# Performance work log

Measured on AMD Instinct MI355X. Metric: run time of the kernel, lower is better.

## Reference

```python
import jax, jax.numpy as jnp
import numpy as np

D_MODEL = 2048
D_FF = 8192
N_EXPERTS = 4
B, S = 2, 2048


def setup_inputs() -> dict:
    key = jax.random.key(0)
    ks = jax.random.split(key, 6)
    scale = 0.02
    return {
        "hidden_states": jax.random.normal(ks[0], (B, S, D_MODEL), dtype=jnp.float32),
        "Wr": jax.random.normal(ks[1], (D_MODEL, N_EXPERTS), dtype=jnp.float32) * scale,
        "br": jnp.zeros((N_EXPERTS,), dtype=jnp.float32),
        "Wg": jax.random.normal(ks[2], (N_EXPERTS, D_MODEL, D_FF), dtype=jnp.float32) * scale,
        "Wu": jax.random.normal(ks[3], (N_EXPERTS, D_MODEL, D_FF), dtype=jnp.float32) * scale,
        "Wd": jax.random.normal(ks[4], (N_EXPERTS, D_FF, D_MODEL), dtype=jnp.float32) * scale,
    }


def reference(hidden_states, Wr, br, Wg, Wu, Wd):
    b, s, d = hidden_states.shape
    x = hidden_states.reshape(-1, d)  # [T, d]

    # Router: top-1 over softmax probabilities
    logits = x @ Wr + br                      # [T, E]
    probs = jax.nn.softmax(logits, axis=-1)   # [T, E]
    top_w, top_idx = jax.lax.top_k(probs, 1)  # [T, 1], [T, 1]

    # Mistral gated MLP per expert, computed densely then selected (same math
    # as masked gather -> expert MLP -> masked_scatter with top-1 routing).
    g = jnp.einsum('td,edf->tef', x, Wg)      # [T, E, f]
    u = jnp.einsum('td,edf->tef', x, Wu)      # [T, E, f]
    h = jax.nn.silu(g) * u                    # [T, E, f]
    y = jnp.einsum('tef,efd->ted', h, Wd)     # [T, E, d]

    sel = jnp.take_along_axis(y, top_idx[:, :, None], axis=1)[:, 0]  # [T, d]
    out = sel * top_w                          # scale by top-1 routing weight
    return out.reshape(b, s, d)
```

## Files before the change

### kernel.cpp

```cpp
#include <hip/hip_runtime.h>

#define T_TOK 4096
#define DM 2048
#define DF 8192
#define NE 4
#define BM 256
#define BN 64
#define GBN 128
#define GBK 64
#define G2BK 32
#define BKO 32
#define MAX_TILES 20
#define PADROWS 256
#define LDK (BKO + 8)

typedef __attribute__((ext_vector_type(8))) short short8;
typedef __attribute__((ext_vector_type(4))) float f32x4;

__device__ __forceinline__ unsigned short f2bf(float f) {
  unsigned int u = __float_as_uint(f);
  u += 0x7fffu + ((u >> 16) & 1u);
  return (unsigned short)(u >> 16);
}

__device__ __forceinline__ void gld_lds16(const unsigned short* g, unsigned short* l) {
  __builtin_amdgcn_global_load_lds(
      (const __attribute__((address_space(1))) unsigned int*)g,
      (__attribute__((address_space(3))) unsigned int*)l, 16, 0, 0);
}

__global__ __launch_bounds__(256) void router_kernel(
    const float* __restrict__ x, const float* __restrict__ Wr,
    const float* __restrict__ br, int* __restrict__ top_idx,
    float* __restrict__ top_w, int* __restrict__ counts) {
  int tok = (blockIdx.x * blockDim.x + threadIdx.x) >> 6;
  int lane = threadIdx.x & 63;
  if (tok >= T_TOK) return;
  const float* xr = x + (size_t)tok * DM;
  float s0 = 0.f, s1 = 0.f, s2 = 0.f, s3 = 0.f;
  for (int j = lane; j < DM; j += 64) {
    float xv = xr[j];
    float4 w = *(const float4*)(Wr + (size_t)j * NE);
    s0 += xv * w.x; s1 += xv * w.y; s2 += xv * w.z; s3 += xv * w.w;
  }
#pragma unroll
  for (int off = 32; off > 0; off >>= 1) {
    s0 += __shfl_xor(s0, off);
    s1 += __shfl_xor(s1, off);
    s2 += __shfl_xor(s2, off);
    s3 += __shfl_xor(s3, off);
  }
  if (lane == 0) {
    float l[NE] = {s0 + br[0], s1 + br[1], s2 + br[2], s3 + br[3]};
    int bi = 0; float bm = l[0];
#pragma unroll
    for (int e = 1; e < NE; e++) if (l[e] > bm) { bm = l[e]; bi = e; }
    float s = 0.f;
#pragma unroll
    for (int e = 0; e < NE; e++) s += __expf(l[e] - bm);
    top_idx[tok] = bi;
    top_w[tok] = 1.0f / s;
    atomicAdd(&counts[bi], 1);
  }
}

__global__ void scan_kernel(const int* __restrict__ counts, int* __restrict__ offs,
                            int* __restrict__ cursors, int* __restrict__ tiles) {
  if (threadIdx.x != 0 || blockIdx.x != 0) return;
  int offv[NE + 1];
  offv[0] = 0;
  for (int e = 0; e < NE; e++) offv[e + 1] = offv[e] + counts[e];
  for (int e = 0; e <= NE; e++) offs[e] = offv[e];
  for (int e = 0; e < NE; e++) cursors[e] = offv[e];
  int nt = 0;
  for (int e = 0; e < NE; e++) {
    int c = counts[e];
    for (int s = 0; s < c; s += BM) {
      tiles[nt * 3 + 0] = e;
      tiles[nt * 3 + 1] = offv[e] + s;
      tiles[nt * 3 + 2] = (c - s < BM) ? (c - s) : BM;
      nt++;
    }
  }
  for (; nt < MAX_TILES; nt++) {
    tiles[nt * 3 + 0] = 0; tiles[nt * 3 + 1] = 0; tiles[nt * 3 + 2] = 0;
  }
}

__global__ __launch_bounds__(256) void scatter_kernel(
    const int* __restrict__ top_idx, int* __restrict__ cursors,
    int* __restrict__ sorted) {
  int t = blockIdx.x * blockDim.x + threadIdx.x;
  if (t >= T_TOK) return;
  int e = top_idx[t];
  int p = atomicAdd(&cursors[e], 1);
  sorted[p] = t;
}

__global__ __launch_bounds__(256) void gather_x_kernel(
    const float* __restrict__ x, const int* __restrict__ sorted,
    unsigned short* __restrict__ xs) {
  const int row = blockIdx.x;
  const int t = threadIdx.x;
  unsigned short* orow = xs + (size_t)row * DM + (t << 3);
  if (row >= T_TOK) {
    short8 z = (short8){0,0,0,0,0,0,0,0};
    *(short8*)orow = z;
    return;
  }
  const float* irow = x + (size_t)sorted[row] * DM + (t << 3);
  float4 a = *(const float4*)irow;
  float4 b = *(const float4*)(irow + 4);
  short8 p;
  p[0] = (short)f2bf(a.x); p[1] = (short)f2bf(a.y);
  p[2] = (short)f2bf(a.z); p[3] = (short)f2bf(a.w);
  p[4] = (short)f2bf(b.x); p[5] = (short)f2bf(b.y);
  p[6] = (short)f2bf(b.z); p[7] = (short)f2bf(b.w);
  *(short8*)orow = p;
}

__global__ __launch_bounds__(256) void transpose_cvt_kernel(
    const float* __restrict__ in, unsigned short* __restrict__ out, int R, int C) {
  __shared__ float tile[64][68];
  const size_t eo = (size_t)blockIdx.z * (size_t)R * (size_t)C;
  const float* inp = in + eo;
  unsigned short* outp = out + eo;
  const int r0 = blockIdx.y << 6, c0 = blockIdx.x << 6;
  const int t = threadIdx.x;
  const int lrow = t >> 4, lcol = (t & 15) << 2;
#pragma unroll
  for (int i = 0; i < 4; i++) {
    float4 v = *(const float4*)(inp + (size_t)(r0 + (i << 4) + lrow) * C + c0 + lcol);
    *(float4*)&tile[(i << 4) + lrow][lcol] = v;
  }
  __syncthreads();
  const int gg = t & 7, cc = t >> 3;
#pragma unroll
  for (int cp = 0; cp < 2; cp++) {
    int c = cc + (cp << 5);
    short8 pv;
#pragma unroll
    for (int i = 0; i < 8; i++) pv[i] = (short)f2bf(tile[(gg << 3) + i][c]);
    *(short8*)(outp + (size_t)(c0 + c) * R + r0 + (gg << 3)) = pv;
  }
}

__global__ __launch_bounds__(512, 2) void gemm1_bf16_kernel(
    const unsigned short* __restrict__ xs, const unsigned short* __restrict__ wg,
    const unsigned short* __restrict__ wu, const int* __restrict__ tiles,
    unsigned short* __restrict__ hbuf) {
  const int slot = blockIdx.x;
  const int e = tiles[slot * 3 + 0];
  const int row0 = tiles[slot * 3 + 1];
  const int nvalid = tiles[slot * 3 + 2];
  if (nvalid == 0) return;
  const int n0 = blockIdx.y * GBN;

  __shared__ __align__(16) unsigned short As[2][BM * GBK];
  __shared__ __align__(16) unsigned short Bg[2][GBN * GBK];
  __shared__ __align__(16) unsigned short Bu[2][GBN * GBK];

  const int t = threadIdx.x;
  const int w = t >> 6, lane = t & 63;
  const int l3 = lane >> 3;
  const int swz = (lane & 7) ^ l3;
  const int lr = lane & 15;
  const int wm = w >> 2, wn = w & 3;

  const unsigned short* wge = wg + (size_t)e * DM * DF;
  const unsigned short* wue = wu + (size_t)e * DM * DF;

  const unsigned short* sA = xs + (size_t)(row0 + (w << 6) + l3) * DM + (swz << 3);
  const unsigned short* sBg = wge + (size_t)(n0 + ((w - 4) << 6) + l3) * DM + (swz << 3);
  const unsigned short* sBu = wue + (size_t)(n0 + ((w - 6) << 6) + l3) * DM + (swz << 3);

  f32x4 accg[8][2], accu[8][2];
#pragma unroll
  for (int mi = 0; mi < 8; mi++)
#pragma unroll
    for (int ni = 0; ni < 2; ni++) {
      accg[mi][ni] = (f32x4){0.f, 0.f, 0.f, 0.f};
      accu[mi][ni] = (f32x4){0.f, 0.f, 0.f, 0.f};
    }

#define G1_STAGE(B, K0)                                                        \
  do {                                                                         \
    if (w < 4) {                                                               \
      unsigned short* d = &As[B][(w << 6) << 6];                               \
      _Pragma("unroll")                                                        \
      for (int j = 0; j < 8; j++)                                              \
        gld_lds16(sA + (size_t)(j << 3) * DM + (K0), d + (j << 9));            \
    } else if (w < 6) {                                                        \
      unsigned short* d = &Bg[B][((w - 4) << 6) << 6];                         \
      _Pragma("unroll")                                                        \
      for (int j = 0; j < 8; j++)                                              \
        gld_lds16(sBg + (size_t)(j << 3) * DM + (K0), d + (j << 9));           \
    } else {                                                                   \
      unsigned short* d = &Bu[B][((w - 6) << 6) << 6];                         \
      _Pragma("unroll")                                                        \
      for (int j = 0; j < 8; j++)                                              \
        gld_lds16(sBu + (size_t)(j << 3) * DM + (K0), d + (j << 9));           \
    }                                                                          \
  } while (0)

#define G1_COMPUTE(B)                                                          \
  do {                                                                         \
    _Pragma("unroll")                                                          \
    for (int h = 0; h < 2; h++) {                                              \
      const int gq = (h << 2) + (lane >> 4);                                   \
      const int g = gq ^ (lr & 7);                                             \
      short8 af[8], bgf[2], buf2[2];                                           \
      _Pragma("unroll")                                                        \
      for (int mi = 0; mi < 8; mi++) {                                         \
        int row = (wm << 7) + (mi << 4) + lr;                                  \
        af[mi] = *(const short8*)&As[B][(row << 6) + (g << 3)];                \
      }                                                                        \
      _Pragma("unroll")                                                        \
      for (int ni = 0; ni < 2; ni++) {                                         \
        int row = (wn << 5) + (ni << 4) + lr;                                  \
        bgf[ni]  = *(const short8*)&Bg[B][(row << 6) + (g << 3)];              \
        buf2[ni] = *(const short8*)&Bu[B][(row << 6) + (g << 3)];              \
      }                                                                        \
      _Pragma("unroll")                                                        \
      for (int mi = 0; mi < 8; mi++)                                           \
        _Pragma("unroll")                                                      \
        for (int ni = 0; ni < 2; ni++) {                                       \
          accg[mi][ni] = __builtin_amdgcn_mfma_f32_16x16x32_bf16(              \
              af[mi], bgf[ni], accg[mi][ni], 0, 0, 0);                         \
          accu[mi][ni] = __builtin_amdgcn_mfma_f32_16x16x32_bf16(              \
              af[mi], buf2[ni], accu[mi][ni], 0, 0, 0);                        \
        }                                                                      \
    }                                                                          \
  } while (0)

  const int NK = DM / GBK;
  int cur = 0;
  G1_STAGE(0, 0);
  __syncthreads();
  for (int kt = 0; kt < NK - 1; ++kt) {
    G1_STAGE(cur ^ 1, (kt + 1) * GBK);
    G1_COMPUTE(cur);
    __syncthreads();
    cur ^= 1;
  }
  G1_COMPUTE(cur);

  const int l4 = (lane >> 4) << 2;
#pragma unroll
  for (int mi = 0; mi < 8; mi++) {
#pragma unroll
    for (int r = 0; r < 4; r++) {
      int lrow = (wm << 7) + (mi << 4) + l4 + r;
      if (lrow < nvalid) {
        size_t base = (size_t)(row0 + lrow) * DF + n0 + (wn << 5) + lr;
#pragma unroll
        for (int ni = 0; ni < 2; ni++) {
          float gv = accg[mi][ni][r];
          float uv = accu[mi][ni][r];
          float hv = (gv / (1.f + __expf(-gv))) * uv;
          hbuf[base + (ni << 4)] = f2bf(hv);
        }
      }
    }
  }
#undef G1_STAGE
#undef G1_COMPUTE
}

__global__ __launch_bounds__(512, 4) void gemm2_bf16_kernel(
    const unsigned short* __restrict__ hbuf, const unsigned short* __restrict__ wd,
    const int* __restrict__ tiles, const int* __restrict__ sorted,
    const float* __restrict__ topw, float* __restrict__ out) {
  const int slot = blockIdx.x;
  const int e = tiles[slot * 3 + 0];
  const int row0 = tiles[slot * 3 + 1];
  const int nvalid = tiles[slot * 3 + 2];
  if (nvalid == 0) return;
  const int n0 = blockIdx.y * GBN;

  __shared__ __align__(16) unsigned short As[2][BM * G2BK];
  __shared__ __align__(16) unsigned short Bs[2][GBN * G2BK];

  const int t = threadIdx.x;
  const int w = t >> 6, lane = t & 63;
  const int lr = lane & 15;
  const int wm = w >> 2, wn = w & 3;

  const int srow = lane >> 2;
  const int sg = (lane & 3) ^ ((lane >> 3) & 3);

  const unsigned short* wde = wd + (size_t)e * DM * DF;
  const unsigned short* sA = hbuf + (size_t)(row0 + (w << 6) + srow) * DF + (sg << 3);
  const unsigned short* sB = wde + (size_t)(n0 + ((w - 4) << 5) + srow) * DF + (sg << 3);

  f32x4 acc[8][2];
#pragma unroll
  for (int mi = 0; mi < 8; mi++)
#pragma unroll
    for (int ni = 0; ni < 2; ni++) acc[mi][ni] = (f32x4){0.f, 0.f, 0.f, 0.f};

#define G2_STAGE(B_, K0)                                                       \
  do {                                                                         \
    if (w < 4) {                                                               \
      _Pragma("unroll")                                                        \
      for (int j = 0; j < 4; j++)                                              \
        gld_lds16(sA + (size_t)(j << 4) * DF + (K0),                           \
                  &As[B_][((w << 2) + j) << 9]);                               \
    } else {                                                                   \
      _Pragma("unroll")                                                        \
      for (int j = 0; j < 2; j++)                                              \
        gld_lds16(sB + (size_t)(j << 4) * DF + (K0),                           \
                  &Bs[B_][(((w - 4) << 1) + j) << 9]);                         \
    }                                                                          \
  } while (0)

#define G2_COMPUTE(B_)                                                         \
  do {                                                                         \
    const int q = lane >> 4;                                                   \
    const int p = q ^ ((lr >> 1) & 3);                                         \
    short8 af[8], bf2[2];                                                      \
    _Pragma("unroll")                                                          \
    for (int mi = 0; mi < 8; mi++) {                                           \
      int row = (wm << 7) + (mi << 4) + lr;                                    \
      af[mi] = *(const short8*)&As[B_][(row << 5) + (p << 3)];                 \
    }                                                                          \
    _Pragma("unroll")                                                          \
    for (int ni = 0; ni < 2; ni++) {                                           \
      int row = (wn << 5) + (ni << 4) + lr;                                    \
      bf2[ni] = *(const short8*)&Bs[B_][(row << 5) + (p << 3)];                \
    }                                                                          \
    _Pragma("unroll")                                                          \
    for (int mi = 0; mi < 8; mi++)                                             \
      _Pragma("unroll")                                                        \
      for (int ni = 0; ni < 2; ni++)                                           \
        acc[mi][ni] = __builtin_amdgcn_mfma_f32_16x16x32_bf16(                 \
            af[mi], bf2[ni], acc[mi][ni], 0, 0, 0);                            \
  } while (0)

  const int NK = DF / G2BK;
  int cur = 0;
  G2_STAGE(0, 0);
  __syncthreads();
  for (int kt = 0; kt < NK - 1; ++kt) {
    G2_STAGE(cur ^ 1, (kt + 1) * G2BK);
    G2_COMPUTE(cur);
    __syncthreads();
    cur ^= 1;
  }
  G2_COMPUTE(cur);

  const int l4 = (lane >> 4) << 2;
#pragma unroll
  for (int mi = 0; mi < 8; mi++) {
#pragma unroll
    for (int r = 0; r < 4; r++) {
      int lrow = (wm << 7) + (mi << 4) + l4 + r;
      if (lrow < nvalid) {
        int tok = sorted[row0 + lrow];
        float wv = topw[tok];
        size_t base = (size_t)tok * DM + n0 + (wn << 5) + lr;
#pragma unroll
        for (int ni = 0; ni < 2; ni++)
          out[base + (ni << 4)] = acc[mi][ni][r] * wv;
      }
    }
  }
#undef G2_STAGE
#undef G2_COMPUTE
}

__global__ __launch_bounds__(512, 4) void gemm1_f32_kernel(
    const float* __restrict__ x, const float* __restrict__ Wg,
    const float* __restrict__ Wu, const int* __restrict__ tiles,
    const int* __restrict__ sorted, unsigned short* __restrict__ hbuf) {
  const int slot = blockIdx.x;
  const int e = tiles[slot * 3 + 0];
  const int row0 = tiles[slot * 3 + 1];
  const int nvalid = tiles[slot * 3 + 2];
  if (nvalid == 0) return;
  const int n0 = blockIdx.y * BN;

  __shared__ __align__(16) unsigned short As[BM][LDK];
  __shared__ __align__(16) unsigned short Bg[BN][LDK];
  __shared__ __align__(16) unsigned short Bu[BN][LDK];

  const int t = threadIdx.x;
  const int arow = t >> 1;
  const int ah = (t & 1) << 4;
  const int atok = (arow < nvalid) ? sorted[row0 + arow] : -1;
  const float* __restrict__ xrow = x + (size_t)(atok >= 0 ? atok : 0) * DM;
  const int bn = t & 63;
  const int bkq = (t >> 6) << 2;

  const size_t eo = (size_t)e * DM * DF;
  const float* __restrict__ Wge = Wg + eo;
  const float* __restrict__ Wue = Wu + eo;

  const int wv = t >> 6, lane = t & 63;
  const int wrow = (wv >> 1) << 6, wcol = (wv & 1) << 5;
  const int lr = lane & 15, lk = (lane >> 4) << 3;

  f32x4 accg[4][2], accu[4][2];
#pragma unroll
  for (int mi = 0; mi < 4; mi++)
#pragma unroll
    for (int ni = 0; ni < 2; ni++) {
      accg[mi][ni] = (f32x4){0.f, 0.f, 0.f, 0.f};
      accu[mi][ni] = (f32x4){0.f, 0.f, 0.f, 0.f};
    }

  for (int k0 = 0; k0 < DM; k0 += BKO) {
#pragma unroll
    for (int j = 0; j < 4; j++) {
      float4 v = make_float4(0.f, 0.f, 0.f, 0.f);
      if (atok >= 0) v = *(const float4*)(xrow + k0 + ah + (j << 2));
      ushort4 pv;
      pv.x = f2bf(v.x); pv.y = f2bf(v.y); pv.z = f2bf(v.z); pv.w = f2bf(v.w);
      *(ushort4*)&As[arow][ah + (j << 2)] = pv;
    }
    {
      const float* pg = Wge + (size_t)(k0 + bkq) * DF + n0 + bn;
      const float* pu = Wue + (size_t)(k0 + bkq) * DF + n0 + bn;
      ushort4 vg, vu;
      vg.x = f2bf(pg[0]);              vu.x = f2bf(pu[0]);
      vg.y = f2bf(pg[(size_t)DF]);     vu.y = f2bf(pu[(size_t)DF]);
      vg.z = f2bf(pg[(size_t)2 * DF]); vu.z = f2bf(pu[(size_t)2 * DF]);
      vg.w = f2bf(pg[(size_t)3 * DF]); vu.w = f2bf(pu[(size_t)3 * DF]);
      *(ushort4*)&Bg[bn][bkq] = vg;
      *(ushort4*)&Bu[bn][bkq] = vu;
    }
    __syncthreads();

    short8 af[4], bgf[2], buf2[2];
#pragma unroll
    for (int mi = 0; mi < 4; mi++)
      af[mi] = *(const short8*)&As[wrow + (mi << 4) + lr][lk];
#pragma unroll
    for (int ni = 0; ni < 2; ni++) {
      bgf[ni]  = *(const short8*)&Bg[wcol + (ni << 4) + lr][lk];
      buf2[ni] = *(const short8*)&Bu[wcol + (ni << 4) + lr][lk];
    }
#pragma unroll
    for (int mi = 0; mi < 4; mi++)
#pragma unroll
      for (int ni = 0; ni < 2; ni++) {
        accg[mi][ni] = __builtin_amdgcn_mfma_f32_16x16x32_bf16(af[mi], bgf[ni], accg[mi][ni], 0, 0, 0);
        accu[mi][ni] = __builtin_amdgcn_mfma_f32_16x16x32_bf16(af[mi], buf2[ni], accu[mi][ni], 0, 0, 0);
      }
    __syncthreads();
  }

  const int l4 = (lane >> 4) << 2;
#pragma unroll
  for (int mi = 0; mi < 4; mi++) {
#pragma unroll
    for (int r = 0; r < 4; r++) {
      int lrow = wrow + (mi << 4) + l4 + r;
      if (lrow < nvalid) {
        size_t base = (size_t)(row0 + lrow) * DF + n0 + wcol + lr;
#pragma unroll
        for (int ni = 0; ni < 2; ni++) {
          float g = accg[mi][ni][r];
          float u = accu[mi][ni][r];
          float hv = (g / (1.f + __expf(-g))) * u;
          hbuf[base + (ni << 4)] = f2bf(hv);
        }
      }
    }
  }
}

__global__ __launch_bounds__(512, 4) void gemm2_f32_kernel(
    const unsigned short* __restrict__ hbuf, const float* __restrict__ Wd,
    const int* __restrict__ tiles, const int* __restrict__ sorted,
    const float* __restrict__ topw, float* __restrict__ out) {
  const int slot = blockIdx.x;
  const int e = tiles[slot * 3 + 0];
  const int row0 = tiles[slot * 3 + 1];
  const int nvalid = tiles[slot * 3 + 2];
  if (nvalid == 0) return;
  const int n0 = blockIdx.y * BN;

  __shared__ __align__(16) unsigned short As[BM][LDK];
  __shared__ __align__(16) unsigned short Bs[BN][LDK];

  const int t = threadIdx.x;
  const int arow = t >> 1;
  const int ah = (t & 1) << 4;
  const int bn = t & 63;
  const int bkq = (t >> 6) << 2;
  const float* __restrict__ Wde = Wd + (size_t)e * DF * DM;

  const int wv = t >> 6, lane = t & 63;
  const int wrow = (wv >> 1) << 6, wcol = (wv & 1) << 5;
  const int lr = lane & 15, lk = (lane >> 4) << 3;

  f32x4 acc[4][2];
#pragma unroll
  for (int mi = 0; mi < 4; mi++)
#pragma unroll
    for (int ni = 0; ni < 2; ni++) acc[mi][ni] = (f32x4){0.f, 0.f, 0.f, 0.f};

  const unsigned short* __restrict__ hrow =
      hbuf + (size_t)(row0 + (arow < nvalid ? arow : 0)) * DF;

  for (int k0 = 0; k0 < DF; k0 += BKO) {
    {
      short8 v0 = (short8){0,0,0,0,0,0,0,0}, v1 = v0;
      if (arow < nvalid) {
        v0 = *(const short8*)(hrow + k0 + ah);
        v1 = *(const short8*)(hrow + k0 + ah + 8);
      }
      *(short8*)&As[arow][ah] = v0;
      *(short8*)&As[arow][ah + 8] = v1;
    }
    {
      const float* pd = Wde + (size_t)(k0 + bkq) * DM + n0 + bn;
      ushort4 vd;
      vd.x = f2bf(pd[0]);
      vd.y = f2bf(pd[(size_t)DM]);
      vd.z = f2bf(pd[(size_t)2 * DM]);
      vd.w = f2bf(pd[(size_t)3 * DM]);
      *(ushort4*)&Bs[bn][bkq] = vd;
    }
    __syncthreads();

    short8 af[4], bf2[2];
#pragma unroll
    for (int mi = 0; mi < 4; mi++)
      af[mi] = *(const short8*)&As[wrow + (mi << 4) + lr][lk];
#pragma unroll
    for (int ni = 0; ni < 2; ni++)
      bf2[ni] = *(const short8*)&Bs[wcol + (ni << 4) + lr][lk];
#pragma unroll
    for (int mi = 0; mi < 4; mi++)
#pragma unroll
      for (int ni = 0; ni < 2; ni++)
        acc[mi][ni] = __builtin_amdgcn_mfma_f32_16x16x32_bf16(af[mi], bf2[ni], acc[mi][ni], 0, 0, 0);
    __syncthreads();
  }

  const int l4 = (lane >> 4) << 2;
#pragma unroll
  for (int mi = 0; mi < 4; mi++) {
#pragma unroll
    for (int r = 0; r < 4; r++) {
      int lrow = wrow + (mi << 4) + l4 + r;
      if (lrow < nvalid) {
        int tok = sorted[row0 + lrow];
        float w = topw[tok];
        size_t base = (size_t)tok * DM + n0 + wcol + lr;
#pragma unroll
        for (int ni = 0; ni < 2; ni++)
          out[base + (ni << 4)] = acc[mi][ni][r] * w;
      }
    }
  }
}

extern "C" void kernel_launch(void* const* d_in, const int* in_sizes, int n_in,
                              void* d_out, int out_size, void* d_ws, size_t ws_size,
                              hipStream_t stream) {
  const float* x  = (const float*)d_in[0];
  const float* Wr = (const float*)d_in[1];
  const float* br = (const float*)d_in[2];
  const float* Wg = (const float*)d_in[3];
  const float* Wu = (const float*)d_in[4];
  const float* Wd = (const float*)d_in[5];
  float* out = (float*)d_out;

  const size_t XS_ELEMS = (size_t)(T_TOK + PADROWS) * DM;
  const size_t HB_ELEMS = (size_t)(T_TOK + PADROWS) * DF;
  const size_t W_ELEMS  = (size_t)NE * DM * DF;
  const size_t NEED = (XS_ELEMS + HB_ELEMS + 3 * W_ELEMS) * 2 + (1 << 20);

  if (ws_size >= NEED) {
    unsigned short* xs = (unsigned short*)d_ws;
    unsigned short* hb = xs + XS_ELEMS;
    unsigned short* wg = hb + HB_ELEMS;
    unsigned short* wu = wg + W_ELEMS;
    unsigned short* wd = wu + W_ELEMS;
    int* meta = (int*)(wd + W_ELEMS);
    int* top_idx = meta;
    int* sorted  = meta + 4096;
    int* counts  = meta + 8192;
    int* offs    = meta + 8196;
    int* cursors = meta + 8201;
    int* tiles   = meta + 8208;
    float* topw  = (float*)(meta + 8320);

    hipMemsetAsync(counts, 0, NE * sizeof(int), stream);
    router_kernel<<<dim3((T_TOK * 64) / 256), 256, 0, stream>>>(x, Wr, br, top_idx, topw, counts);
    scan_kernel<<<1, 1, 0, stream>>>(counts, offs, cursors, tiles);
    scatter_kernel<<<dim3(T_TOK / 256), 256, 0, stream>>>(top_idx, cursors, sorted);
    gather_x_kernel<<<dim3(T_TOK + PADROWS), 256, 0, stream>>>(x, sorted, xs);
    transpose_cvt_kernel<<<dim3(DF / 64, DM / 64, NE), 256, 0, stream>>>(Wg, wg, DM, DF);
    transpose_cvt_kernel<<<dim3(DF / 64, DM / 64, NE), 256, 0, stream>>>(Wu, wu, DM, DF);
    transpose_cvt_kernel<<<dim3(DM / 64, DF / 64, NE), 256, 0, stream>>>(Wd, wd, DF, DM);
    gemm1_bf16_kernel<<<dim3(MAX_TILES, DF / GBN), 512, 0, stream>>>(xs, wg, wu, tiles, hb);
    gemm2_bf16_kernel<<<dim3(MAX_TILES, DM / GBN), 512, 0, stream>>>(hb, wd, tiles, sorted, topw, out);
  } else {
    const size_t H_BYTES = (size_t)T_TOK * DF * 2;
    unsigned short* hbuf = (unsigned short*)d_ws;
    int* meta = (int*)((char*)d_ws + H_BYTES);
    int* top_idx = meta;
    int* sorted  = meta + 4096;
    int* counts  = meta + 8192;
    int* offs    = meta + 8196;
    int* cursors = meta + 8201;
    int* tiles   = meta + 8208;
    float* topw  = (float*)(meta + 8320);

    hipMemsetAsync(counts, 0, NE * sizeof(int), stream);
    router_kernel<<<dim3((T_TOK * 64) / 256), 256, 0, stream>>>(x, Wr, br, top_idx, topw, counts);
    scan_kernel<<<1, 1, 0, stream>>>(counts, offs, cursors, tiles);
    scatter_kernel<<<dim3(T_TOK / 256), 256, 0, stream>>>(top_idx, cursors, sorted);
    gemm1_f32_kernel<<<dim3(MAX_TILES, DF / BN), 512, 0, stream>>>(x, Wg, Wu, tiles, sorted, hbuf);
    gemm2_f32_kernel<<<dim3(MAX_TILES, DM / BN), 512, 0, stream>>>(hbuf, Wd, tiles, sorted, topw, out);
  }
}
```

Measured before the change: 896.6 us.

## Keep two async stage loads in flight with explicit vmcnt waits in both GEMMs

Restructures the main loops of both the gate/up GEMM and the down GEMM so two K-stages are prefetched before compute. Each iteration waits with a partial s_waitcnt vmcnt count instead of a full __syncthreads drain, so the next stage's global loads stay in flight during MFMA compute. It also raises wave priority around the compute block with s_setprio. The hand-tuned vmcnt counts depend on how many loads each wave issues per stage (different for waves below and above 4 in GEMM2), and a wrong count would cause a race.

```diff
diff --git a/kernel.cpp b/kernel.cpp
--- a/kernel.cpp
+++ b/kernel.cpp
@@ -234,16 +234,24 @@
   } while (0)
 
   const int NK = DM / GBK;
-  int cur = 0;
   G1_STAGE(0, 0);
-  __syncthreads();
-  for (int kt = 0; kt < NK - 1; ++kt) {
-    G1_STAGE(cur ^ 1, (kt + 1) * GBK);
-    G1_COMPUTE(cur);
-    __syncthreads();
-    cur ^= 1;
-  }
-  G1_COMPUTE(cur);
+  G1_STAGE(1, GBK);
+  for (int kt = 0; kt < NK; ++kt) {
+    if (kt < NK - 1) {
+      asm volatile("s_waitcnt vmcnt(8)" ::: "memory");
+    } else {
+      asm volatile("s_waitcnt vmcnt(0)" ::: "memory");
+    }
+    __builtin_amdgcn_sched_barrier(0);
+    __builtin_amdgcn_s_barrier();
+    asm volatile("" ::: "memory");
+    __builtin_amdgcn_s_setprio(1);
+    G1_COMPUTE(kt & 1);
+    __builtin_amdgcn_s_setprio(0);
+    __builtin_amdgcn_s_barrier();
+    asm volatile("" ::: "memory");
+    if (kt + 2 < NK) G1_STAGE(kt & 1, (kt + 2) * GBK);
+  }
 
   const int l4 = (lane >> 4) << 2;
 #pragma unroll
@@ -338,16 +346,25 @@
   } while (0)
 
   const int NK = DF / G2BK;
-  int cur = 0;
   G2_STAGE(0, 0);
-  __syncthreads();
-  for (int kt = 0; kt < NK - 1; ++kt) {
-    G2_STAGE(cur ^ 1, (kt + 1) * G2BK);
-    G2_COMPUTE(cur);
-    __syncthreads();
-    cur ^= 1;
-  }
-  G2_COMPUTE(cur);
+  G2_STAGE(1, G2BK);
+  for (int kt = 0; kt < NK; ++kt) {
+    if (kt < NK - 1) {
+      if (w < 4) asm volatile("s_waitcnt vmcnt(4)" ::: "memory");
+      else       asm volatile("s_waitcnt vmcnt(2)" ::: "memory");
+    } else {
+      asm volatile("s_waitcnt vmcnt(0)" ::: "memory");
+    }
+    __builtin_amdgcn_sched_barrier(0);
+    __builtin_amdgcn_s_barrier();
+    asm volatile("" ::: "memory");
+    __builtin_amdgcn_s_setprio(1);
+    G2_COMPUTE(kt & 1);
+    __builtin_amdgcn_s_setprio(0);
+    __builtin_amdgcn_s_barrier();
+    asm volatile("" ::: "memory");
+    if (kt + 2 < NK) G2_STAGE(kt & 1, (kt + 2) * G2BK);
+  }
 
   const int l4 = (lane >> 4) << 2;
 #pragma unroll
```

Measured after the change: 945.4 us. +5.4%, slower.

## Rework gemm1 mainloop into 4-stage LDS pipeline with split loads and setprio

Applied to the files above, without the earlier changes.

Rewrites the gate/up GEMM main loop to use a four-buffer LDS ring with K-step 32 instead of a double buffer with K-step 64. Each iteration uses one barrier with an explicit vmcnt wait, and issues the next stage's async global-to-LDS loads in two halves, interleaved between the gate and up MFMA groups. MFMA blocks run at raised wave priority via s_setprio. The goal is to hide global load latency and remove the extra barrier per step. It relies on hand-counted vmcnt values and a new swizzle layout, which risks correctness and register pressure.

```diff
diff --git a/kernel.cpp b/kernel.cpp
--- a/kernel.cpp
+++ b/kernel.cpp
@@ -7,7 +7,7 @@
 #define BM 256
 #define BN 64
 #define GBN 128
-#define GBK 64
+#define G1BK 32
 #define G2BK 32
 #define BKO 32
 #define MAX_TILES 20
@@ -156,23 +156,24 @@
   if (nvalid == 0) return;
   const int n0 = blockIdx.y * GBN;
 
-  __shared__ __align__(16) unsigned short As[2][BM * GBK];
-  __shared__ __align__(16) unsigned short Bg[2][GBN * GBK];
-  __shared__ __align__(16) unsigned short Bu[2][GBN * GBK];
+  __shared__ __align__(16) unsigned short As[4][BM * G1BK];
+  __shared__ __align__(16) unsigned short Bg[4][GBN * G1BK];
+  __shared__ __align__(16) unsigned short Bu[4][GBN * G1BK];
 
   const int t = threadIdx.x;
   const int w = t >> 6, lane = t & 63;
-  const int l3 = lane >> 3;
-  const int swz = (lane & 7) ^ l3;
   const int lr = lane & 15;
   const int wm = w >> 2, wn = w & 3;
 
+  const int srow = lane >> 2;
+  const int sg = (lane & 3) ^ ((lane >> 3) & 3);
+
   const unsigned short* wge = wg + (size_t)e * DM * DF;
   const unsigned short* wue = wu + (size_t)e * DM * DF;
 
-  const unsigned short* sA = xs + (size_t)(row0 + (w << 6) + l3) * DM + (swz << 3);
-  const unsigned short* sBg = wge + (size_t)(n0 + ((w - 4) << 6) + l3) * DM + (swz << 3);
-  const unsigned short* sBu = wue + (size_t)(n0 + ((w - 6) << 6) + l3) * DM + (swz << 3);
+  const unsigned short* sA = xs + (size_t)(row0 + (w << 6) + srow) * DM + (sg << 3);
+  const unsigned short* sBg = wge + (size_t)(n0 + ((w - 4) << 6) + srow) * DM + (sg << 3);
+  const unsigned short* sBu = wue + (size_t)(n0 + ((w - 6) << 6) + srow) * DM + (sg << 3);
 
   f32x4 accg[8][2], accu[8][2];
 #pragma unroll
@@ -183,67 +184,75 @@
       accu[mi][ni] = (f32x4){0.f, 0.f, 0.f, 0.f};
     }
 
-#define G1_STAGE(B, K0)                                                        \
+#define G1_STAGE_HALF(B_, K0, h)                                               \
   do {                                                                         \
-    if (w < 4) {                                                               \
-      unsigned short* d = &As[B][(w << 6) << 6];                               \
-      _Pragma("unroll")                                                        \
-      for (int j = 0; j < 8; j++)                                              \
-        gld_lds16(sA + (size_t)(j << 3) * DM + (K0), d + (j << 9));            \
-    } else if (w < 6) {                                                        \
-      unsigned short* d = &Bg[B][((w - 4) << 6) << 6];                         \
-      _Pragma("unroll")                                                        \
-      for (int j = 0; j < 8; j++)                                              \
-        gld_lds16(sBg + (size_t)(j << 3) * DM + (K0), d + (j << 9));           \
-    } else {                                                                   \
-      unsigned short* d = &Bu[B][((w - 6) << 6) << 6];                         \
-      _Pragma("unroll")                                                        \
-      for (int j = 0; j < 8; j++)                                              \
-        gld_lds16(sBu + (size_t)(j << 3) * DM + (K0), d + (j << 9));           \
+    _Pragma("unroll")                                                          \
+    for (int j = (h) * 2; j < (h) * 2 + 2; j++) {                              \
+      if (w < 4)                                                               \
+        gld_lds16(sA + (size_t)(j << 4) * DM + (K0),                           \
+                  &As[B_][((w << 2) + j) << 9]);                               \
+      else if (w < 6)                                                          \
+        gld_lds16(sBg + (size_t)(j << 4) * DM + (K0),                          \
+                  &Bg[B_][(((w - 4) << 2) + j) << 9]);                         \
+      else                                                                     \
+        gld_lds16(sBu + (size_t)(j << 4) * DM + (K0),                          \
+                  &Bu[B_][(((w - 6) << 2) + j) << 9]);                         \
     }                                                                          \
   } while (0)
 
-#define G1_COMPUTE(B)                                                          \
-  do {                                                                         \
-    _Pragma("unroll")                                                          \
-    for (int h = 0; h < 2; h++) {                                              \
-      const int gq = (h << 2) + (lane >> 4);                                   \
-      const int g = gq ^ (lr & 7);                                             \
-      short8 af[8], bgf[2], buf2[2];                                           \
-      _Pragma("unroll")                                                        \
-      for (int mi = 0; mi < 8; mi++) {                                         \
-        int row = (wm << 7) + (mi << 4) + lr;                                  \
-        af[mi] = *(const short8*)&As[B][(row << 6) + (g << 3)];                \
-      }                                                                        \
-      _Pragma("unroll")                                                        \
-      for (int ni = 0; ni < 2; ni++) {                                         \
-        int row = (wn << 5) + (ni << 4) + lr;                                  \
-        bgf[ni]  = *(const short8*)&Bg[B][(row << 6) + (g << 3)];              \
-        buf2[ni] = *(const short8*)&Bu[B][(row << 6) + (g << 3)];              \
-      }                                                                        \
-      _Pragma("unroll")                                                        \
-      for (int mi = 0; mi < 8; mi++)                                           \
-        _Pragma("unroll")                                                      \
-        for (int ni = 0; ni < 2; ni++) {                                       \
-          accg[mi][ni] = __builtin_amdgcn_mfma_f32_16x16x32_bf16(              \
-              af[mi], bgf[ni], accg[mi][ni], 0, 0, 0);                         \
-          accu[mi][ni] = __builtin_amdgcn_mfma_f32_16x16x32_bf16(              \
-              af[mi], buf2[ni], accu[mi][ni], 0, 0, 0);                        \
-        }                                                                      \
-    }                                                                          \
-  } while (0)
-
-  const int NK = DM / GBK;
-  int cur = 0;
-  G1_STAGE(0, 0);
-  __syncthreads();
-  for (int kt = 0; kt < NK - 1; ++kt) {
-    G1_STAGE(cur ^ 1, (kt + 1) * GBK);
-    G1_COMPUTE(cur);
-    __syncthreads();
-    cur ^= 1;
-  }
-  G1_COMPUTE(cur);
+  const int NK = DM / G1BK;
+  G1_STAGE_HALF(0, 0, 0); G1_STAGE_HALF(0, 0, 1);
+  G1_STAGE_HALF(1, G1BK, 0); G1_STAGE_HALF(1, G1BK, 1);
+  G1_STAGE_HALF(2, 2 * G1BK, 0); G1_STAGE_HALF(2, 2 * G1BK, 1);
+
+#pragma unroll 4
+  for (int kt = 0; kt < NK; ++kt) {
+    const int rb = kt & 3;
+    const int nb = (kt + 3) & 3;
+    if (kt < NK - 2)       asm volatile("s_waitcnt vmcnt(8)" ::: "memory");
+    else if (kt == NK - 2) asm volatile("s_waitcnt vmcnt(4)" ::: "memory");
+    else                   asm volatile("s_waitcnt vmcnt(0)" ::: "memory");
+    __builtin_amdgcn_sched_barrier(0);
+    __builtin_amdgcn_s_barrier();
+    __builtin_amdgcn_sched_barrier(0);
+
+    const int q = lane >> 4;
+    const int p_ = q ^ ((lr >> 1) & 3);
+    short8 af[8], bb[2];
+#pragma unroll
+    for (int mi = 0; mi < 8; mi++) {
+      int row = (wm << 7) + (mi << 4) + lr;
+      af[mi] = *(const short8*)&As[rb][(row << 5) + (p_ << 3)];
+    }
+#pragma unroll
+    for (int ni = 0; ni < 2; ni++) {
+      int row = (wn << 5) + (ni << 4) + lr;
+      bb[ni] = *(const short8*)&Bg[rb][(row << 5) + (p_ << 3)];
+    }
+    if (kt + 3 < NK) G1_STAGE_HALF(nb, (kt + 3) * G1BK, 0);
+    __builtin_amdgcn_s_setprio(1);
+#pragma unroll
+    for (int mi = 0; mi < 8; mi++)
+#pragma unroll
+      for (int ni = 0; ni < 2; ni++)
+        accg[mi][ni] = __builtin_amdgcn_mfma_f32_16x16x32_bf16(
+            af[mi], bb[ni], accg[mi][ni], 0, 0, 0);
+    __builtin_amdgcn_s_setprio(0);
+#pragma unroll
+    for (int ni = 0; ni < 2; ni++) {
+      int row = (wn << 5) + (ni << 4) + lr;
+      bb[ni] = *(const short8*)&Bu[rb][(row << 5) + (p_ << 3)];
+    }
+    if (kt + 3 < NK) G1_STAGE_HALF(nb, (kt + 3) * G1BK, 1);
+    __builtin_amdgcn_s_setprio(1);
+#pragma unroll
+    for (int mi = 0; mi < 8; mi++)
+#pragma unroll
+      for (int ni = 0; ni < 2; ni++)
+        accu[mi][ni] = __builtin_amdgcn_mfma_f32_16x16x32_bf16(
+            af[mi], bb[ni], accu[mi][ni], 0, 0, 0);
+    __builtin_amdgcn_s_setprio(0);
+  }
 
   const int l4 = (lane >> 4) << 2;
 #pragma unroll
@@ -263,8 +272,7 @@
       }
     }
   }
-#undef G1_STAGE
-#undef G1_COMPUTE
+#undef G1_STAGE_HALF
 }
 
 __global__ __launch_bounds__(512, 4) void gemm2_bf16_kernel(
```

Measured after the change: 961.0 us. 7.2% more time.
